# Performance work log

Measured on AMD Instinct MI355X. Metric: run time of the kernel, lower is better.

Reference implementation:

```python
import jax, jax.numpy as jnp
import numpy as np

DIM = 1024
HEADS = 16
HD = DIM // HEADS            # 64
MLP = 4 * DIM                # 4096
IN_OUT = MLP + 3 * DIM       # 7168, in_proj out dim
OUT_IN = MLP + DIM           # 5120, out_proj in dim
OUT_OUT = 2 * DIM            # 2048, out_proj out dim
R = 2                        # residual PQ levels
K = 64                       # codebook size
NCB = HEADS                  # num_codebooks = num_heads * codebooks_ratio
IN_CLUSTERS = HEADS * (IN_OUT // DIM)                 # 112
OUT_CLUSTERS = HEADS * max(1, OUT_OUT // OUT_IN)      # 16
SUB_IN = DIM // NCB          # 64
SUB_OUT = OUT_IN // NCB      # 320
EPS = 1e-5


def setup_inputs() -> dict:
    key = jax.random.key(0)
    k1, k2, k3, k4, k5 = jax.random.split(key, 5)
    B, N = 4, 1024
    x = jax.random.normal(k1, (B, N, DIM), jnp.float32)
    in_codebooks = jax.random.normal(k2, (R, IN_CLUSTERS, NCB, K, SUB_IN), jnp.float32) * 0.02
    in_indices = jax.random.randint(k3, (R, IN_OUT, NCB), 0, K, jnp.int32)
    out_codebooks = jax.random.normal(k4, (R, OUT_CLUSTERS, NCB, K, SUB_OUT), jnp.float32) * 0.02
    out_indices = jax.random.randint(k5, (R, OUT_OUT, NCB), 0, K, jnp.int32)
    return {"x": x, "in_codebooks": in_codebooks, "in_indices": in_indices,
            "out_codebooks": out_codebooks, "out_indices": out_indices}


def _decode_weight(cb, idx):
    """Decode RPQ weight. cb: (R, n_clusters, n_codebooks, K, sub), idx: (R, O, n_codebooks).
    Returns dense weight (O, n_codebooks*sub)."""
    Rr, nclust, C, _, sub = cb.shape
    O = idx.shape[1]
    cluster = jnp.arange(O) // (O // nclust)                       # per-row cluster id
    w = cb[jnp.arange(Rr)[:, None, None],
           cluster[None, :, None],
           jnp.arange(C)[None, None, :],
           idx]                                                    # (R, O, C, sub)
    return w.sum(0).reshape(O, C * sub)


def reference(x, in_codebooks, in_indices, out_codebooks, out_indices):
    B, N, C = x.shape
    res = x
    # LayerNorm without affine
    mu = x.mean(-1, keepdims=True)
    var = x.var(-1, keepdims=True)
    xn = (x - mu) * jax.lax.rsqrt(var + EPS)
    # in_proj: dequant + GEMM
    Win = _decode_weight(in_codebooks, in_indices)                 # (IN_OUT, DIM)
    h = jnp.einsum('bnc,oc->bno', xn, Win)                         # (B, N, IN_OUT)
    xm, q, k, v = jnp.split(h, [MLP, MLP + DIM, MLP + 2 * DIM], axis=-1)
    q = q.reshape(B, N, HEADS, HD).transpose(0, 2, 1, 3)
    k = k.reshape(B, N, HEADS, HD).transpose(0, 2, 1, 3)
    v = v.reshape(B, N, HEADS, HD).transpose(0, 2, 1, 3)
    scale = HD ** -0.5
    attn = jax.nn.softmax(jnp.einsum('bhqd,bhkd->bhqk', q, k) * scale, axis=-1)
    xa = jnp.einsum('bhqk,bhkd->bhqd', attn, v).transpose(0, 2, 1, 3).reshape(B, N, C)
    # out_proj: dequant + GEMM on concatenated [mlp, attn]
    Wout = _decode_weight(out_codebooks, out_indices)              # (OUT_OUT, OUT_IN)
    o = jnp.einsum('bnc,oc->bno', jnp.concatenate([xm, xa], axis=-1), Wout)
    x_mlp, x_attn = o[..., :DIM], o[..., DIM:]
    return x_mlp + x_attn + res
```

## Files before the change

### kernel.cpp

```cpp
#include <hip/hip_runtime.h>
#include <hip/hip_bf16.h>

typedef float f32x4 __attribute__((ext_vector_type(4)));
typedef short short8 __attribute__((ext_vector_type(8)));

#define LDH 7168
#define MFMA16(d, x, y) d = __builtin_amdgcn_mfma_f32_16x16x32_bf16(x, y, d, 0, 0, 0)

__device__ __forceinline__ void async_ld16(const void* g, void* l) {
  __builtin_amdgcn_global_load_lds(
      (const __attribute__((address_space(1))) unsigned int*)g,
      (__attribute__((address_space(3))) unsigned int*)l, 16, 0, 0);
}

__device__ __forceinline__ float bf2f(unsigned short u) {
  union { unsigned int i; float f; } c; c.i = ((unsigned int)u) << 16; return c.f;
}

__device__ __forceinline__ ushort4 pack_bf16x4(float4 v) {
  ushort4 u;
  __hip_bfloat16 b;
  b = __float2bfloat16(v.x); u.x = *(unsigned short*)&b;
  b = __float2bfloat16(v.y); u.y = *(unsigned short*)&b;
  b = __float2bfloat16(v.z); u.z = *(unsigned short*)&b;
  b = __float2bfloat16(v.w); u.w = *(unsigned short*)&b;
  return u;
}

__global__ __launch_bounds__(256) void decode_win_k(const float* __restrict__ cb,
                                                    const int* __restrict__ idx,
                                                    __hip_bfloat16* __restrict__ Win) {
  const int o = blockIdx.x;
  const int cluster = o >> 6;
  const int c = threadIdx.x >> 4;
  const int s4 = (threadIdx.x & 15) * 4;
  const int k0 = idx[o * 16 + c];
  const int k1 = idx[(7168 + o) * 16 + c];
  const float4 v0 = *(const float4*)&cb[((((size_t)cluster) * 16 + c) * 64 + k0) * 64 + s4];
  const float4 v1 = *(const float4*)&cb[((((size_t)(112 + cluster)) * 16 + c) * 64 + k1) * 64 + s4];
  float4 v; v.x = v0.x + v1.x; v.y = v0.y + v1.y; v.z = v0.z + v1.z; v.w = v0.w + v1.w;
  *(ushort4*)&Win[(size_t)o * 1024 + c * 64 + s4] = pack_bf16x4(v);
}

__global__ __launch_bounds__(256) void decode_weff_k(const float* __restrict__ cb,
                                                     const int* __restrict__ idx,
                                                     __hip_bfloat16* __restrict__ W) {
  const int o = blockIdx.x;
  const int cl1 = o >> 7, cl2 = cl1 + 8;
  for (int e4 = threadIdx.x * 4; e4 < 5120; e4 += 1024) {
    const int c = e4 / 320, s = e4 - c * 320;
    float4 acc = {0.f, 0.f, 0.f, 0.f};
    #pragma unroll
    for (int r = 0; r < 2; ++r) {
      const int ka = idx[((size_t)r * 2048 + o) * 16 + c];
      const int kb = idx[((size_t)r * 2048 + o + 1024) * 16 + c];
      const float4 va = *(const float4*)&cb[((((size_t)r * 16 + cl1) * 16 + c) * 64 + ka) * 320 + s];
      const float4 vb = *(const float4*)&cb[((((size_t)r * 16 + cl2) * 16 + c) * 64 + kb) * 320 + s];
      acc.x += va.x + vb.x; acc.y += va.y + vb.y; acc.z += va.z + vb.z; acc.w += va.w + vb.w;
    }
    *(ushort4*)&W[(size_t)o * 5120 + e4] = pack_bf16x4(acc);
  }
}

__global__ __launch_bounds__(256) void ln_k(const float* __restrict__ x,
                                            __hip_bfloat16* __restrict__ xn) {
  const int row = blockIdx.x;
  const float4 v = ((const float4*)(x + (size_t)row * 1024))[threadIdx.x];
  float s = v.x + v.y + v.z + v.w;
  float s2 = v.x * v.x + v.y * v.y + v.z * v.z + v.w * v.w;
  #pragma unroll
  for (int off = 32; off > 0; off >>= 1) {
    s += __shfl_down(s, off, 64);
    s2 += __shfl_down(s2, off, 64);
  }
  __shared__ float red[8];
  if ((threadIdx.x & 63) == 0) { red[threadIdx.x >> 6] = s; red[4 + (threadIdx.x >> 6)] = s2; }
  __syncthreads();
  s = red[0] + red[1] + red[2] + red[3];
  s2 = red[4] + red[5] + red[6] + red[7];
  const float mu = s * (1.f / 1024.f);
  const float rstd = rsqrtf(s2 * (1.f / 1024.f) - mu * mu + 1e-5f);
  float4 nv;
  nv.x = (v.x - mu) * rstd; nv.y = (v.y - mu) * rstd;
  nv.z = (v.z - mu) * rstd; nv.w = (v.w - mu) * rstd;
  *(ushort4*)(xn + (size_t)row * 1024 + threadIdx.x * 4) = pack_bf16x4(nv);
}

__global__ __launch_bounds__(512, 2) void gemm1_k(const __hip_bfloat16* __restrict__ A,
                                                  const __hip_bfloat16* __restrict__ B,
                                                  __hip_bfloat16* __restrict__ C,
                                                  __hip_bfloat16* __restrict__ vT) {
  __shared__ ushort sm[65536];
  const int tid = threadIdx.x;
  const int lane = tid & 63, wid = tid >> 6;
  const int g = lane >> 4, r16 = lane & 15;
  const int wr = wid >> 2, wc = wid & 3;

  const int x = blockIdx.x & 7, local = blockIdx.x >> 3;
  const int mb = (x >> 1) * 4 + local / 14;
  const int nb = (x & 1) * 14 + local % 14;
  const int m0 = mb * 256, n0 = nb * 256;

  auto stageA = [&](int kt, int base) {
    #pragma unroll
    for (int i = 0; i < 4; ++i) {
      const int c = i * 512 + tid;
      const int lc = c ^ (((c >> 5) & 1) << 1);
      const int row = lc >> 3, col = (lc & 7) * 8;
      async_ld16(&A[(size_t)(m0 + row) * 1024 + kt * 64 + col], &sm[base + c * 8]);
    }
  };
  auto stageB = [&](int kt, int base) {
    #pragma unroll
    for (int i = 0; i < 4; ++i) {
      const int c = i * 512 + tid;
      const int lc = c ^ (((c >> 5) & 1) << 1);
      const int row = lc >> 3, col = (lc & 7) * 8;
      async_ld16(&B[(size_t)(n0 + row) * 1024 + kt * 64 + col], &sm[base + 16384 + c * 8]);
    }
  };
  auto rdA = [&](int base, int mm, int kk) -> short8 {
    const int row = wr * 128 + mm * 16 + r16;
    int e = row * 64 + kk * 32 + g * 8;
    e ^= ((row >> 2) & 1) << 4;
    return *(const short8*)&sm[base + e];
  };
  auto rdB = [&](int base, int nn, int kk) -> short8 {
    const int row = wc * 64 + nn * 16 + r16;
    int e = row * 64 + kk * 32 + g * 8;
    e ^= ((row >> 2) & 1) << 4;
    return *(const short8*)&sm[base + 16384 + e];
  };

  f32x4 acc[8][4] = {};

  stageA(0, 0); stageB(0, 0);
  asm volatile("s_waitcnt vmcnt(0)" ::: "memory");
  __builtin_amdgcn_s_barrier();
  __builtin_amdgcn_sched_barrier(0);

  auto tile_body = [&](int kt, int base, int nbase) {
    short8 a0[4][2], a1[4][2], b0[2][2], b1[2][2];
    #pragma unroll
    for (int mm = 0; mm < 4; ++mm) { a0[mm][0] = rdA(base, mm, 0); a0[mm][1] = rdA(base, mm, 1); }
    #pragma unroll
    for (int nn = 0; nn < 2; ++nn) { b0[nn][0] = rdB(base, nn, 0); b0[nn][1] = rdB(base, nn, 1); }
    if (kt + 1 < 16) stageA(kt + 1, nbase);
    __builtin_amdgcn_s_setprio(1);
    #pragma unroll
    for (int mm = 0; mm < 4; ++mm)
      #pragma unroll
      for (int nn = 0; nn < 2; ++nn) {
        MFMA16(acc[mm][nn], a0[mm][0], b0[nn][0]);
        MFMA16(acc[mm][nn], a0[mm][1], b0[nn][1]);
      }
    __builtin_amdgcn_s_setprio(0);
    __builtin_amdgcn_s_barrier();
    #pragma unroll
    for (int nn = 0; nn < 2; ++nn) { b1[nn][0] = rdB(base, 2 + nn, 0); b1[nn][1] = rdB(base, 2 + nn, 1); }
    if (kt + 1 < 16) stageB(kt + 1, nbase);
    __builtin_amdgcn_s_setprio(1);
    #pragma unroll
    for (int mm = 0; mm < 4; ++mm)
      #pragma unroll
      for (int nn = 0; nn < 2; ++nn) {
        MFMA16(acc[mm][2 + nn], a0[mm][0], b1[nn][0]);
        MFMA16(acc[mm][2 + nn], a0[mm][1], b1[nn][1]);
      }
    __builtin_amdgcn_s_setprio(0);
    __builtin_amdgcn_s_barrier();
    #pragma unroll
    for (int mm = 0; mm < 4; ++mm) { a1[mm][0] = rdA(base, 4 + mm, 0); a1[mm][1] = rdA(base, 4 + mm, 1); }
    __builtin_amdgcn_s_setprio(1);
    #pragma unroll
    for (int mm = 0; mm < 4; ++mm)
      #pragma unroll
      for (int nn = 0; nn < 2; ++nn) {
        MFMA16(acc[4 + mm][2 + nn], a1[mm][0], b1[nn][0]);
        MFMA16(acc[4 + mm][2 + nn], a1[mm][1], b1[nn][1]);
      }
    __builtin_amdgcn_s_setprio(0);
    __builtin_amdgcn_s_barrier();
    __builtin_amdgcn_s_setprio(1);
    #pragma unroll
    for (int mm = 0; mm < 4; ++mm)
      #pragma unroll
      for (int nn = 0; nn < 2; ++nn) {
        MFMA16(acc[4 + mm][nn], a1[mm][0], b0[nn][0]);
        MFMA16(acc[4 + mm][nn], a1[mm][1], b0[nn][1]);
      }
    __builtin_amdgcn_s_setprio(0);
    asm volatile("s_waitcnt vmcnt(0) lgkmcnt(0)" ::: "memory");
    __builtin_amdgcn_s_barrier();
    __builtin_amdgcn_sched_barrier(0);
  };

  for (int kt = 0; kt < 16; kt += 2) {
    tile_body(kt, 0, 32768);
    tile_body(kt + 1, 32768, 0);
  }

  if (n0 < 6144) {
    #pragma unroll
    for (int mm = 0; mm < 8; ++mm)
      #pragma unroll
      for (int nn = 0; nn < 4; ++nn)
        #pragma unroll
        for (int r = 0; r < 4; ++r) {
          const int m = m0 + wr * 128 + mm * 16 + g * 4 + r;
          const int o = n0 + wc * 64 + nn * 16 + r16;
          C[(size_t)m * LDH + o] = __float2bfloat16(acc[mm][nn][r]);
        }
  } else {
    #pragma unroll
    for (int mm = 0; mm < 8; ++mm)
      #pragma unroll
      for (int nn = 0; nn < 4; ++nn)
        #pragma unroll
        for (int r = 0; r < 4; ++r) {
          const int m = m0 + wr * 128 + mm * 16 + g * 4 + r;
          const int o = n0 + wc * 64 + nn * 16 + r16;
          const int b_ = m >> 10;
          vT[((size_t)b_ * 1024 + (o - 6144)) * 1024 + (m & 1023)] = __float2bfloat16(acc[mm][nn][r]);
        }
  }
}

__global__ __launch_bounds__(256) void attn_k(const __hip_bfloat16* __restrict__ h,
                                              const __hip_bfloat16* __restrict__ vT,
                                              __hip_bfloat16* __restrict__ xa) {
  const int qt = blockIdx.x, head = blockIdx.y, b = blockIdx.z;
  const int tid = threadIdx.x;
  const int lane = tid & 63, w = tid >> 6;
  const int g = lane >> 4, r16 = lane & 15;

  __shared__ __align__(16) __hip_bfloat16 Ks[2][64 * 64];
  __shared__ __align__(16) __hip_bfloat16 Vs[2][64 * 64];
  __shared__ __align__(16) __hip_bfloat16 P[4][16][72];

  const __hip_bfloat16* Kg = h + (size_t)(b * 1024) * LDH + 5120 + head * 64;
  const __hip_bfloat16* Vg = vT + ((size_t)b * 1024 + head * 64) * 1024;

  const size_t qrow = (size_t)(b * 1024 + qt * 64 + w * 16 + r16);
  short8 aq0 = *(const short8*)&h[qrow * LDH + 4096 + head * 64 + g * 8];
  short8 aq1 = *(const short8*)&h[qrow * LDH + 4096 + head * 64 + 32 + g * 8];

  auto stage = [&](int buf, int t) {
    #pragma unroll
    for (int i = 0; i < 2; ++i) {
      const int c_lin = i * 256 + tid;
      const int row = c_lin >> 3;
      const int c_log = (c_lin & 7) ^ (row & 7);
      async_ld16(&Kg[(size_t)(t * 64 + row) * LDH + c_log * 8], &Ks[buf][c_lin * 8]);
    }
    #pragma unroll
    for (int i = 0; i < 2; ++i) {
      const int c_lin = i * 256 + tid;
      const int row = c_lin >> 3;
      const int c_log = (c_lin & 7) ^ (row & 7);
      async_ld16(&Vg[(size_t)row * 1024 + t * 64 + c_log * 8], &Vs[buf][c_lin * 8]);
    }
  };

  f32x4 o_acc[4] = {};
  float l_r[4] = {0.f, 0.f, 0.f, 0.f};

  stage(0, 0);
  for (int t = 0; t < 16; ++t) {
    const int buf = t & 1;
    if (t + 1 < 16) {
      stage(buf ^ 1, t + 1);
      asm volatile("s_waitcnt vmcnt(4)" ::: "memory");
    } else {
      asm volatile("s_waitcnt vmcnt(0)" ::: "memory");
    }
    __builtin_amdgcn_s_barrier();
    __builtin_amdgcn_sched_barrier(0);

    f32x4 s_acc[4] = {};
    #pragma unroll
    for (int nn = 0; nn < 4; ++nn) {
      const int row = nn * 16 + r16;
      short8 bk0 = *(const short8*)&Ks[buf][row * 64 + ((g ^ (row & 7)) * 8)];
      short8 bk1 = *(const short8*)&Ks[buf][row * 64 + (((g + 4) ^ (row & 7)) * 8)];
      s_acc[nn] = __builtin_amdgcn_mfma_f32_16x16x32_bf16(aq0, bk0, s_acc[nn], 0, 0, 0);
      s_acc[nn] = __builtin_amdgcn_mfma_f32_16x16x32_bf16(aq1, bk1, s_acc[nn], 0, 0, 0);
    }

    #pragma unroll
    for (int nn = 0; nn < 4; ++nn)
      #pragma unroll
      for (int r = 0; r < 4; ++r) {
        const float p = __expf(s_acc[nn][r] * 0.125f);
        s_acc[nn][r] = p;
        l_r[r] += p;
      }

    #pragma unroll
    for (int nn = 0; nn < 4; ++nn)
      #pragma unroll
      for (int r = 0; r < 4; ++r)
        P[w][g * 4 + r][nn * 16 + r16] = __float2bfloat16(s_acc[nn][r]);
    short8 ap0 = *(const short8*)&P[w][r16][g * 8];
    short8 ap1 = *(const short8*)&P[w][r16][32 + g * 8];

    #pragma unroll
    for (int nn = 0; nn < 4; ++nn) {
      const int row = nn * 16 + r16;
      short8 bv0 = *(const short8*)&Vs[buf][row * 64 + ((g ^ (row & 7)) * 8)];
      short8 bv1 = *(const short8*)&Vs[buf][row * 64 + (((g + 4) ^ (row & 7)) * 8)];
      o_acc[nn] = __builtin_amdgcn_mfma_f32_16x16x32_bf16(ap0, bv0, o_acc[nn], 0, 0, 0);
      o_acc[nn] = __builtin_amdgcn_mfma_f32_16x16x32_bf16(ap1, bv1, o_acc[nn], 0, 0, 0);
    }
    __builtin_amdgcn_s_barrier();
    __builtin_amdgcn_sched_barrier(0);
  }

  #pragma unroll
  for (int r = 0; r < 4; ++r) {
    float l = l_r[r];
    #pragma unroll
    for (int off = 1; off < 16; off <<= 1) l += __shfl_xor(l, off, 64);
    const float inv = 1.0f / l;
    const size_t mrow = (size_t)(b * 1024 + qt * 64 + w * 16 + g * 4 + r);
    #pragma unroll
    for (int nn = 0; nn < 4; ++nn)
      xa[mrow * 1024 + head * 64 + nn * 16 + r16] = __float2bfloat16(o_acc[nn][r] * inv);
  }
}

__global__ __launch_bounds__(512, 2) void gemm2_k(const __hip_bfloat16* __restrict__ h,
                                                  const __hip_bfloat16* __restrict__ xa,
                                                  const __hip_bfloat16* __restrict__ W,
                                                  const float* __restrict__ res,
                                                  __hip_bfloat16* __restrict__ p0,
                                                  __hip_bfloat16* __restrict__ p1,
                                                  __hip_bfloat16* __restrict__ p2,
                                                  float* __restrict__ out) {
  __shared__ ushort sm[65536];
  const int tid = threadIdx.x;
  const int lane = tid & 63, wid = tid >> 6;
  const int g = lane >> 4, r16 = lane & 15;
  const int wr = wid >> 2, wc = wid & 3;

  int bid = blockIdx.x;
  bid = (bid & 7) * 8 + (bid >> 3);
  const int mb = bid >> 2, nb = bid & 3;
  const int m0 = mb * 256, n0 = nb * 256;
  const int z = blockIdx.y;
  const int kt0 = z * 20, ktEnd = kt0 + 20;

  auto stageA = [&](int kt, int base) {
    const __hip_bfloat16* Ab; size_t lda; int kc;
    if (kt < 64) { Ab = h;  lda = LDH;  kc = kt * 64; }
    else         { Ab = xa; lda = 1024; kc = kt * 64 - 4096; }
    #pragma unroll
    for (int i = 0; i < 4; ++i) {
      const int c = i * 512 + tid;
      const int lc = c ^ (((c >> 5) & 1) << 1);
      const int row = lc >> 3, col = (lc & 7) * 8;
      async_ld16(&Ab[(size_t)(m0 + row) * lda + kc + col], &sm[base + c * 8]);
    }
  };
  auto stageB = [&](int kt, int base) {
    #pragma unroll
    for (int i = 0; i < 4; ++i) {
      const int c = i * 512 + tid;
      const int lc = c ^ (((c >> 5) & 1) << 1);
      const int row = lc >> 3, col = (lc & 7) * 8;
      async_ld16(&W[(size_t)(n0 + row) * 5120 + kt * 64 + col], &sm[base + 16384 + c * 8]);
    }
  };
  auto rdA = [&](int base, int mm, int kk) -> short8 {
    const int row = wr * 128 + mm * 16 + r16;
    int e = row * 64 + kk * 32 + g * 8;
    e ^= ((row >> 2) & 1) << 4;
    return *(const short8*)&sm[base + e];
  };
  auto rdB = [&](int base, int nn, int kk) -> short8 {
    const int row = wc * 64 + nn * 16 + r16;
    int e = row * 64 + kk * 32 + g * 8;
    e ^= ((row >> 2) & 1) << 4;
    return *(const short8*)&sm[base + 16384 + e];
  };

  f32x4 acc[8][4] = {};

  stageA(kt0, 0); stageB(kt0, 0);
  asm volatile("s_waitcnt vmcnt(0)" ::: "memory");
  __builtin_amdgcn_s_barrier();
  __builtin_amdgcn_sched_barrier(0);

  auto tile_body = [&](int kt, int base, int nbase) {
    short8 a0[4][2], a1[4][2], b0[2][2], b1[2][2];
    #pragma unroll
    for (int mm = 0; mm < 4; ++mm) { a0[mm][0] = rdA(base, mm, 0); a0[mm][1] = rdA(base, mm, 1); }
    #pragma unroll
    for (int nn = 0; nn < 2; ++nn) { b0[nn][0] = rdB(base, nn, 0); b0[nn][1] = rdB(base, nn, 1); }
    if (kt + 1 < ktEnd) stageA(kt + 1, nbase);
    __builtin_amdgcn_s_setprio(1);
    #pragma unroll
    for (int mm = 0; mm < 4; ++mm)
      #pragma unroll
      for (int nn = 0; nn < 2; ++nn) {
        MFMA16(acc[mm][nn], a0[mm][0], b0[nn][0]);
        MFMA16(acc[mm][nn], a0[mm][1], b0[nn][1]);
      }
    __builtin_amdgcn_s_setprio(0);
    __builtin_amdgcn_s_barrier();
    #pragma unroll
    for (int nn = 0; nn < 2; ++nn) { b1[nn][0] = rdB(base, 2 + nn, 0); b1[nn][1] = rdB(base, 2 + nn, 1); }
    if (kt + 1 < ktEnd) stageB(kt + 1, nbase);
    __builtin_amdgcn_s_setprio(1);
    #pragma unroll
    for (int mm = 0; mm < 4; ++mm)
      #pragma unroll
      for (int nn = 0; nn < 2; ++nn) {
        MFMA16(acc[mm][2 + nn], a0[mm][0], b1[nn][0]);
        MFMA16(acc[mm][2 + nn], a0[mm][1], b1[nn][1]);
      }
    __builtin_amdgcn_s_setprio(0);
    __builtin_amdgcn_s_barrier();
    #pragma unroll
    for (int mm = 0; mm < 4; ++mm) { a1[mm][0] = rdA(base, 4 + mm, 0); a1[mm][1] = rdA(base, 4 + mm, 1); }
    __builtin_amdgcn_s_setprio(1);
    #pragma unroll
    for (int mm = 0; mm < 4; ++mm)
      #pragma unroll
      for (int nn = 0; nn < 2; ++nn) {
        MFMA16(acc[4 + mm][2 + nn], a1[mm][0], b1[nn][0]);
        MFMA16(acc[4 + mm][2 + nn], a1[mm][1], b1[nn][1]);
      }
    __builtin_amdgcn_s_setprio(0);
    __builtin_amdgcn_s_barrier();
    __builtin_amdgcn_s_setprio(1);
    #pragma unroll
    for (int mm = 0; mm < 4; ++mm)
      #pragma unroll
      for (int nn = 0; nn < 2; ++nn) {
        MFMA16(acc[4 + mm][nn], a1[mm][0], b0[nn][0]);
        MFMA16(acc[4 + mm][nn], a1[mm][1], b0[nn][1]);
      }
    __builtin_amdgcn_s_setprio(0);
    asm volatile("s_waitcnt vmcnt(0) lgkmcnt(0)" ::: "memory");
    __builtin_amdgcn_s_barrier();
    __builtin_amdgcn_sched_barrier(0);
  };

  for (int kt = kt0; kt < ktEnd; kt += 2) {
    tile_body(kt, 0, 32768);
    tile_body(kt + 1, 32768, 0);
  }

  __hip_bfloat16* pz = (z == 0) ? p0 : (z == 1) ? p1 : p2;
  #pragma unroll
  for (int mm = 0; mm < 8; ++mm)
    #pragma unroll
    for (int nn = 0; nn < 4; ++nn)
      #pragma unroll
      for (int r = 0; r < 4; ++r) {
        const int m = m0 + wr * 128 + mm * 16 + g * 4 + r;
        const int n = n0 + wc * 64 + nn * 16 + r16;
        if (z == 3) out[(size_t)m * 1024 + n] = acc[mm][nn][r] + res[(size_t)m * 1024 + n];
        else        pz[(size_t)m * 1024 + n] = __float2bfloat16(acc[mm][nn][r]);
      }
}

__global__ __launch_bounds__(256) void reduce_k(const __hip_bfloat16* __restrict__ p0,
                                                const __hip_bfloat16* __restrict__ p1,
                                                const __hip_bfloat16* __restrict__ p2,
                                                float* __restrict__ out) {
  const size_t i4 = (size_t)blockIdx.x * 256 + threadIdx.x;
  float4 o = ((const float4*)out)[i4];
  const ushort4 a0 = ((const ushort4*)p0)[i4];
  const ushort4 a1 = ((const ushort4*)p1)[i4];
  const ushort4 a2 = ((const ushort4*)p2)[i4];
  o.x += bf2f(a0.x) + bf2f(a1.x) + bf2f(a2.x);
  o.y += bf2f(a0.y) + bf2f(a1.y) + bf2f(a2.y);
  o.z += bf2f(a0.z) + bf2f(a1.z) + bf2f(a2.z);
  o.w += bf2f(a0.w) + bf2f(a1.w) + bf2f(a2.w);
  ((float4*)out)[i4] = o;
}

extern "C" void kernel_launch(void* const* d_in, const int* in_sizes, int n_in,
                              void* d_out, int out_size, void* d_ws, size_t ws_size,
                              hipStream_t stream) {
  (void)in_sizes; (void)n_in; (void)out_size; (void)ws_size;
  const float* x      = (const float*)d_in[0];
  const float* in_cb  = (const float*)d_in[1];
  const int*   in_idx = (const int*)d_in[2];
  const float* out_cb = (const float*)d_in[3];
  const int*   out_idx= (const int*)d_in[4];
  float* out = (float*)d_out;
  char* ws = (char*)d_ws;

  __hip_bfloat16* Win  = (__hip_bfloat16*)(ws);
  __hip_bfloat16* Weff = (__hip_bfloat16*)(ws + 14680064);
  __hip_bfloat16* xn   = (__hip_bfloat16*)(ws + 25165824);
  __hip_bfloat16* h    = (__hip_bfloat16*)(ws + 33554432);
  __hip_bfloat16* vT   = (__hip_bfloat16*)(ws + 92274688);
  __hip_bfloat16* xa   = (__hip_bfloat16*)(ws + 100663296);

  __hip_bfloat16* pk0 = Win;
  __hip_bfloat16* pk1 = xn;
  __hip_bfloat16* pk2 = vT;

  decode_win_k<<<dim3(7168), dim3(256), 0, stream>>>(in_cb, in_idx, Win);
  decode_weff_k<<<dim3(1024), dim3(256), 0, stream>>>(out_cb, out_idx, Weff);
  ln_k<<<dim3(4096), dim3(256), 0, stream>>>(x, xn);
  gemm1_k<<<dim3(448), dim3(512), 0, stream>>>(xn, Win, h, vT);
  attn_k<<<dim3(16, 16, 4), dim3(256), 0, stream>>>(h, vT, xa);
  gemm2_k<<<dim3(64, 4), dim3(512), 0, stream>>>(h, xa, Weff, x, pk0, pk1, pk2, out);
  reduce_k<<<dim3(4096), dim3(256), 0, stream>>>(pk0, pk1, pk2, out);
}
```

Measured before the change: 226.3 us.

## Split attention KV range across two blocks and combine partial outputs

Attention now splits the 16 key tiles into two halves handled by separate blocks, doubling the grid from 1024 to 2048 blocks. Each half writes unnormalized bf16 partial outputs and row sums, and a new combine kernel adds them and normalizes. This targets low occupancy and the long serial loop in attention. The cost is an extra launch and extra memory traffic. The residual add also moves from gemm2 into the reduce kernel. Partial sums can be combined without per-half max rescaling only because the softmax as written never subtracts a running max.

```diff
diff --git a/kernel.cpp b/kernel.cpp
--- a/kernel.cpp
+++ b/kernel.cpp
@@ -228,8 +228,11 @@
 
 __global__ __launch_bounds__(256) void attn_k(const __hip_bfloat16* __restrict__ h,
                                               const __hip_bfloat16* __restrict__ vT,
-                                              __hip_bfloat16* __restrict__ xa) {
-  const int qt = blockIdx.x, head = blockIdx.y, b = blockIdx.z;
+                                              __hip_bfloat16* __restrict__ po0,
+                                              __hip_bfloat16* __restrict__ po1,
+                                              float* __restrict__ lbuf) {
+  const int qt = blockIdx.x & 15, kvs = blockIdx.x >> 4;
+  const int head = blockIdx.y, b = blockIdx.z;
   const int tid = threadIdx.x;
   const int lane = tid & 63, w = tid >> 6;
   const int g = lane >> 4, r16 = lane & 15;
@@ -265,11 +268,12 @@
   f32x4 o_acc[4] = {};
   float l_r[4] = {0.f, 0.f, 0.f, 0.f};
 
-  stage(0, 0);
-  for (int t = 0; t < 16; ++t) {
-    const int buf = t & 1;
-    if (t + 1 < 16) {
-      stage(buf ^ 1, t + 1);
+  const int t0 = kvs * 8;
+  stage(0, t0);
+  for (int tt = 0; tt < 8; ++tt) {
+    const int buf = tt & 1;
+    if (tt + 1 < 8) {
+      stage(buf ^ 1, t0 + tt + 1);
       asm volatile("s_waitcnt vmcnt(4)" ::: "memory");
     } else {
       asm volatile("s_waitcnt vmcnt(0)" ::: "memory");
@@ -316,23 +320,42 @@
     __builtin_amdgcn_sched_barrier(0);
   }
 
+  __hip_bfloat16* po = kvs ? po1 : po0;
   #pragma unroll
   for (int r = 0; r < 4; ++r) {
     float l = l_r[r];
     #pragma unroll
     for (int off = 1; off < 16; off <<= 1) l += __shfl_xor(l, off, 64);
-    const float inv = 1.0f / l;
     const size_t mrow = (size_t)(b * 1024 + qt * 64 + w * 16 + g * 4 + r);
     #pragma unroll
     for (int nn = 0; nn < 4; ++nn)
-      xa[mrow * 1024 + head * 64 + nn * 16 + r16] = __float2bfloat16(o_acc[nn][r] * inv);
-  }
+      po[mrow * 1024 + head * 64 + nn * 16 + r16] = __float2bfloat16(o_acc[nn][r]);
+    if (r16 == 0) lbuf[(mrow * 16 + head) * 2 + kvs] = l;
+  }
+}
+
+__global__ __launch_bounds__(256) void combine_k(const __hip_bfloat16* __restrict__ po0,
+                                                 const float* __restrict__ lbuf,
+                                                 __hip_bfloat16* __restrict__ xa) {
+  const int row = blockIdx.x;
+  const int e4 = threadIdx.x * 4;
+  const int head = e4 >> 6;
+  const float l = lbuf[(((size_t)row) * 16 + head) * 2 + 0]
+                + lbuf[(((size_t)row) * 16 + head) * 2 + 1];
+  const float inv = 1.0f / l;
+  const ushort4 a = *(const ushort4*)&po0[(size_t)row * 1024 + e4];
+  const ushort4 bb = *(const ushort4*)&xa[(size_t)row * 1024 + e4];
+  float4 v;
+  v.x = (bf2f(a.x) + bf2f(bb.x)) * inv;
+  v.y = (bf2f(a.y) + bf2f(bb.y)) * inv;
+  v.z = (bf2f(a.z) + bf2f(bb.z)) * inv;
+  v.w = (bf2f(a.w) + bf2f(bb.w)) * inv;
+  *(ushort4*)&xa[(size_t)row * 1024 + e4] = pack_bf16x4(v);
 }
 
 __global__ __launch_bounds__(512, 2) void gemm2_k(const __hip_bfloat16* __restrict__ h,
                                                   const __hip_bfloat16* __restrict__ xa,
                                                   const __hip_bfloat16* __restrict__ W,
-                                                  const float* __restrict__ res,
                                                   __hip_bfloat16* __restrict__ p0,
                                                   __hip_bfloat16* __restrict__ p1,
                                                   __hip_bfloat16* __restrict__ p2,
@@ -461,7 +484,7 @@
       for (int r = 0; r < 4; ++r) {
         const int m = m0 + wr * 128 + mm * 16 + g * 4 + r;
         const int n = n0 + wc * 64 + nn * 16 + r16;
-        if (z == 3) out[(size_t)m * 1024 + n] = acc[mm][nn][r] + res[(size_t)m * 1024 + n];
+        if (z == 3) out[(size_t)m * 1024 + n] = acc[mm][nn][r];
         else        pz[(size_t)m * 1024 + n] = __float2bfloat16(acc[mm][nn][r]);
       }
 }
@@ -469,16 +492,18 @@
 __global__ __launch_bounds__(256) void reduce_k(const __hip_bfloat16* __restrict__ p0,
                                                 const __hip_bfloat16* __restrict__ p1,
                                                 const __hip_bfloat16* __restrict__ p2,
+                                                const float* __restrict__ res,
                                                 float* __restrict__ out) {
   const size_t i4 = (size_t)blockIdx.x * 256 + threadIdx.x;
   float4 o = ((const float4*)out)[i4];
+  const float4 rr = ((const float4*)res)[i4];
   const ushort4 a0 = ((const ushort4*)p0)[i4];
   const ushort4 a1 = ((const ushort4*)p1)[i4];
   const ushort4 a2 = ((const ushort4*)p2)[i4];
-  o.x += bf2f(a0.x) + bf2f(a1.x) + bf2f(a2.x);
-  o.y += bf2f(a0.y) + bf2f(a1.y) + bf2f(a2.y);
-  o.z += bf2f(a0.z) + bf2f(a1.z) + bf2f(a2.z);
-  o.w += bf2f(a0.w) + bf2f(a1.w) + bf2f(a2.w);
+  o.x += rr.x + bf2f(a0.x) + bf2f(a1.x) + bf2f(a2.x);
+  o.y += rr.y + bf2f(a0.y) + bf2f(a1.y) + bf2f(a2.y);
+  o.z += rr.z + bf2f(a0.z) + bf2f(a1.z) + bf2f(a2.z);
+  o.w += rr.w + bf2f(a0.w) + bf2f(a1.w) + bf2f(a2.w);
   ((float4*)out)[i4] = o;
 }
 
@@ -501,6 +526,8 @@
   __hip_bfloat16* vT   = (__hip_bfloat16*)(ws + 92274688);
   __hip_bfloat16* xa   = (__hip_bfloat16*)(ws + 100663296);
 
+  __hip_bfloat16* po0  = Win;
+  float*          lbuf = (float*)xn;
   __hip_bfloat16* pk0 = Win;
   __hip_bfloat16* pk1 = xn;
   __hip_bfloat16* pk2 = vT;
@@ -509,7 +536,8 @@
   decode_weff_k<<<dim3(1024), dim3(256), 0, stream>>>(out_cb, out_idx, Weff);
   ln_k<<<dim3(4096), dim3(256), 0, stream>>>(x, xn);
   gemm1_k<<<dim3(448), dim3(512), 0, stream>>>(xn, Win, h, vT);
-  attn_k<<<dim3(16, 16, 4), dim3(256), 0, stream>>>(h, vT, xa);
-  gemm2_k<<<dim3(64, 4), dim3(512), 0, stream>>>(h, xa, Weff, x, pk0, pk1, pk2, out);
-  reduce_k<<<dim3(4096), dim3(256), 0, stream>>>(pk0, pk1, pk2, out);
-}
+  attn_k<<<dim3(32, 16, 4), dim3(256), 0, stream>>>(h, vT, po0, xa, lbuf);
+  combine_k<<<dim3(4096), dim3(256), 0, stream>>>(po0, lbuf, xa);
+  gemm2_k<<<dim3(64, 4), dim3(512), 0, stream>>>(h, xa, Weff, pk0, pk1, pk2, out);
+  reduce_k<<<dim3(4096), dim3(256), 0, stream>>>(pk0, pk1, pk2, x, out);
+}
```

Result: faster. 202.9 us (-10.3%).
